# Kernel optimization log

Measured on AMD Instinct MI355X. Metric: run time of the kernel, lower is better.

Reference implementation:

```python
import jax, jax.numpy as jnp
import numpy as np

T = 2048      # num_tokens == max_seq_len
D = 4096      # d_in
H = 32        # num_heads
G = 8         # num_kv_groups
HD = 128      # head_dim
GS = H // G   # group_size = 4
EPS = 1e-6


def _make_rope(t, hd):
    inv_freq = 1.0 / (10000.0 ** (np.arange(0, hd, 2, dtype=np.float64) / hd))
    freqs = np.outer(np.arange(t, dtype=np.float64), inv_freq)      # [T, HD/2]
    emb = np.concatenate([freqs, freqs], axis=-1)                   # [T, HD]
    return (jnp.asarray(np.cos(emb), jnp.float32),
            jnp.asarray(np.sin(emb), jnp.float32))


def setup_inputs() -> dict:
    key = jax.random.key(0)
    ks = jax.random.split(key, 6)
    x = jax.random.normal(ks[0], (T, D), jnp.float32)
    # causal mask: True = masked (upper triangle above diagonal)
    mask = jnp.triu(jnp.ones((T, T), jnp.bool_), k=1)
    cos, sin = _make_rope(T, HD)
    s = 0.02
    Wq = jax.random.normal(ks[1], (D, H * HD), jnp.float32) * s
    Wk = jax.random.normal(ks[2], (D, G * HD), jnp.float32) * s
    Wv = jax.random.normal(ks[3], (D, G * HD), jnp.float32) * s
    Wo = jax.random.normal(ks[4], (H * HD, D), jnp.float32) * s
    qn_w = jnp.ones((HD,), jnp.float32)
    kn_w = jnp.ones((HD,), jnp.float32)
    return {"x": x, "mask": mask, "cos": cos, "sin": sin,
            "Wq": Wq, "Wk": Wk, "Wv": Wv, "Wo": Wo,
            "qn_w": qn_w, "kn_w": kn_w}


def _rmsnorm(u, w):
    # normalize over head_dim (last axis), eps inside sqrt
    var = jnp.mean(jnp.square(u), axis=-1, keepdims=True)
    return u * jax.lax.rsqrt(var + EPS) * w


def _rope(u, cos, sin):
    # rotate-half RoPE; u: [heads, T, HD], cos/sin: [T, HD]
    hd = u.shape[-1]
    u1, u2 = u[..., : hd // 2], u[..., hd // 2:]
    rot = jnp.concatenate([-u2, u1], axis=-1)
    return u * cos[None] + rot * sin[None]


def reference(x, mask, cos, sin, Wq, Wk, Wv, Wo, qn_w, kn_w):
    t = x.shape[0]
    q = (x @ Wq).reshape(t, H, HD).transpose(1, 0, 2)   # [H, T, HD]
    k = (x @ Wk).reshape(t, G, HD).transpose(1, 0, 2)   # [G, T, HD]
    v = (x @ Wv).reshape(t, G, HD).transpose(1, 0, 2)   # [G, T, HD]
    q = _rmsnorm(q, qn_w)
    k = _rmsnorm(k, kn_w)
    q = _rope(q, cos, sin)
    k = _rope(k, cos, sin)
    # GQA expansion: repeat_interleave along head axis
    k = jnp.repeat(k, GS, axis=0)                       # [H, T, HD]
    v = jnp.repeat(v, GS, axis=0)                       # [H, T, HD]
    scores = jnp.einsum('hqd,hkd->hqk', q, k) / (HD ** 0.5)
    scores = jnp.where(mask[None], -jnp.inf, scores)
    w = jax.nn.softmax(scores, axis=-1)
    attn = jnp.einsum('hqk,hkd->hqd', w, v)             # [H, T, HD]
    attn = attn.transpose(1, 0, 2).reshape(t, H * HD)
    return attn @ Wo
```

## Files before the change

kernel.cpp:

```cpp
#include <hip/hip_runtime.h>

#define T_ 2048
#define D_ 4096
#define H_ 32
#define G_ 8
#define HD_ 128

typedef float f32x4 __attribute__((ext_vector_type(4)));
typedef __bf16 bf16x8 __attribute__((ext_vector_type(8)));
typedef unsigned short u16x8 __attribute__((ext_vector_type(8)));
typedef unsigned short u16x4 __attribute__((ext_vector_type(4)));

__device__ __forceinline__ unsigned short f2bf(float f) {
  unsigned u = __builtin_bit_cast(unsigned, f);
  u += 0x7FFFu + ((u >> 16) & 1u);
  return (unsigned short)(u >> 16);
}
__device__ __forceinline__ float bf2f(unsigned short h) {
  return __builtin_bit_cast(float, (unsigned)h << 16);
}

__device__ __forceinline__ void gload_lds16(const unsigned short* g, unsigned short* l) {
  __builtin_amdgcn_global_load_lds((const __attribute__((address_space(1))) void*)g,
                                   (__attribute__((address_space(3))) void*)l, 16, 0, 0);
}

__global__ __launch_bounds__(256) void convert_bf16(const float* __restrict__ in,
                                                    unsigned short* __restrict__ out) {
  const size_t i = ((size_t)blockIdx.x * 256 + threadIdx.x) * 8;
  float4 a = *(const float4*)(in + i);
  float4 b = *(const float4*)(in + i + 4);
  u16x8 o;
  o[0] = f2bf(a.x); o[1] = f2bf(a.y); o[2] = f2bf(a.z); o[3] = f2bf(a.w);
  o[4] = f2bf(b.x); o[5] = f2bf(b.y); o[6] = f2bf(b.z); o[7] = f2bf(b.w);
  *(u16x8*)(out + i) = o;
}

__global__ __launch_bounds__(256) void transpose_convert(const float* __restrict__ Wm,
                                                         unsigned short* __restrict__ Wt,
                                                         int R, int C) {
  __shared__ float tile[64][65];
  const int r0 = blockIdx.x * 64, c0 = blockIdx.y * 64;
  const int lr4 = threadIdx.x >> 6, lc = threadIdx.x & 63;
#pragma unroll
  for (int i = 0; i < 16; ++i) {
    int r = i * 4 + lr4;
    tile[r][lc] = Wm[(size_t)(r0 + r) * C + c0 + lc];
  }
  __syncthreads();
#pragma unroll
  for (int i = 0; i < 16; ++i) {
    int r = i * 4 + lr4;
    Wt[(size_t)(c0 + r) * R + r0 + lc] = f2bf(tile[lc][r]);
  }
}

__global__ __launch_bounds__(256) void transpose_v(const unsigned short* __restrict__ v,
                                                   unsigned short* __restrict__ vt, int stride) {
  __shared__ unsigned short tile[64][65];
  const int t0 = blockIdx.x * 64, d0 = blockIdx.y * 64, g = blockIdx.z;
  const int lr4 = threadIdx.x >> 6, lc = threadIdx.x & 63;
#pragma unroll
  for (int i = 0; i < 16; ++i) {
    int r = i * 4 + lr4;
    tile[r][lc] = v[(size_t)(t0 + r) * stride + g * HD_ + d0 + lc];
  }
  __syncthreads();
#pragma unroll
  for (int i = 0; i < 16; ++i) {
    int r = i * 4 + lr4;
    vt[((size_t)g * HD_ + d0 + r) * T_ + t0 + lc] = tile[lc][r];
  }
}

__global__ __launch_bounds__(256) void norm_rope(const unsigned short* __restrict__ raw,
                                                 int stride,
                                                 unsigned short* __restrict__ outp,
                                                 const float* __restrict__ w,
                                                 const float* __restrict__ cs,
                                                 const float* __restrict__ sn, int NH) {
  const int row = blockIdx.x * 4 + (threadIdx.x >> 6);
  const int lane = threadIdx.x & 63;
  const int t = row / NH, h = row - t * NH;
  const unsigned short* src = raw + (size_t)t * stride + h * HD_;
  float u1 = bf2f(src[lane]);
  float u2 = bf2f(src[lane + 64]);
  float ss = u1 * u1 + u2 * u2;
#pragma unroll
  for (int m = 1; m < 64; m <<= 1) ss += __shfl_xor(ss, m);
  float rr = rsqrtf(ss * (1.f / 128.f) + 1e-6f);
  float c = cs[(size_t)t * HD_ + lane];
  float s = sn[(size_t)t * HD_ + lane];
  float a = u1 * rr * w[lane];
  float b = u2 * rr * w[lane + 64];
  unsigned short* dst = outp + ((size_t)h * T_ + t) * HD_;
  dst[lane]      = f2bf(a * c - b * s);
  dst[lane + 64] = f2bf(b * c + a * s);
}

template <int NF, int F0, int F1>
__device__ __forceinline__ void mfma_g(f32x4 (&acc)[4][NF], bf16x8 (&af)[4][2],
                                       bf16x8 (&bf)[NF][2]) {
  __builtin_amdgcn_s_setprio(1);
#pragma unroll
  for (int fm = 0; fm < 4; ++fm)
#pragma unroll
    for (int fn = F0; fn < F1; ++fn) {
      f32x4 a = acc[fm][fn];
      a = __builtin_amdgcn_mfma_f32_16x16x32_bf16(af[fm][0], bf[fn][0], a, 0, 0, 0);
      a = __builtin_amdgcn_mfma_f32_16x16x32_bf16(af[fm][1], bf[fn][1], a, 0, 0, 0);
      acc[fm][fn] = a;
    }
  __builtin_amdgcn_s_setprio(0);
}

template <int NF, int OUTF32>
__global__ __launch_bounds__(512, 4) void gemm3(const unsigned short* __restrict__ A,
                                                const unsigned short* __restrict__ Bt,
                                                void* __restrict__ Cv, int M, int N,
                                                int K, int LDA) {
  constexpr int BN = NF * 64;
  constexpr int BBUF = NF * 4096;
  __shared__ __align__(16) unsigned short lds[16384 + 2 * BBUF];
  const int tid = threadIdx.x;
  const int wid = tid >> 6, lane = tid & 63;
  const int lr = lane & 15, lhi = lane >> 4;
  const int wr = wid >> 2, wcn = wid & 3;

  int flat = blockIdx.y * gridDim.x + blockIdx.x;
  int nwg = gridDim.x * gridDim.y;
  int swz = (flat & 7) * (nwg >> 3) + (flat >> 3);
  const int brow = (swz & 15) * 128;
  const int bcol = (swz >> 4) * BN;

  const int nt = K >> 6;

  f32x4 acc[4][NF];
#pragma unroll
  for (int b = 0; b < 4; ++b)
#pragma unroll
    for (int c = 0; c < NF; ++c) acc[b][c] = (f32x4){0.f, 0.f, 0.f, 0.f};

  const int t8 = tid >> 3;
  const int srcCol = ((tid & 7) ^ (t8 & 7)) * 8;
  auto stageA = [&](int d, int u, int ktp) {
    gload_lds16(A + (size_t)(brow + u * 64 + t8) * LDA + ktp * 64 + srcCol,
                &lds[d * 8192 + u * 4096 + tid * 8]);
  };
  auto stageB = [&](int d, int v, int ktp) {
    gload_lds16(Bt + (size_t)(bcol + v * 64 + t8) * LDA + ktp * 64 + srcCol,
                &lds[16384 + d * BBUF + v * 4096 + tid * 8]);
  };

  bf16x8 af[4][2], bf[NF][2];
  auto readA = [&](int d) {
#pragma unroll
    for (int fm = 0; fm < 4; ++fm) {
      int row = wr * 64 + fm * 16 + lr;
      int base = d * 8192 + row * 64;
      int sw = (row & 7) << 3;
      af[fm][0] = *(const bf16x8*)&lds[base + ((lhi * 8) ^ sw)];
      af[fm][1] = *(const bf16x8*)&lds[base + ((32 + lhi * 8) ^ sw)];
    }
  };
  auto readBf = [&](int d, int fn, bf16x8 (&slot)[2]) {
    int row = wcn * (16 * NF) + fn * 16 + lr;
    int base = 16384 + d * BBUF + row * 64;
    int sw = (row & 7) << 3;
    slot[0] = *(const bf16x8*)&lds[base + ((lhi * 8) ^ sw)];
    slot[1] = *(const bf16x8*)&lds[base + ((32 + lhi * 8) ^ sw)];
  };

  stageA(0, 0, 0); stageA(0, 1, 0);
#pragma unroll
  for (int v = 0; v < NF; ++v) stageB(0, v, 0);
  stageA(1, 0, 1); stageA(1, 1, 1);
  asm volatile("s_waitcnt vmcnt(2)" ::: "memory");
  __builtin_amdgcn_s_barrier();

  for (int t = 0; t < nt; ++t) {
    const int d = t & 1, dn = d ^ 1;
    if constexpr (NF == 3) {
      readA(d); readBf(d, 0, bf[0]); readBf(d, 1, bf[1]);
      if (t + 1 < nt) { stageB(dn, 0, t + 1); stageB(dn, 1, t + 1); stageB(dn, 2, t + 1); }
      __builtin_amdgcn_s_barrier();
      mfma_g<NF, 0, 2>(acc, af, bf);
      __builtin_amdgcn_s_barrier();
      readBf(d, 2, bf[2]);
      if (t + 2 < nt) { stageA(d, 0, t + 2); stageA(d, 1, t + 2); }
      __builtin_amdgcn_s_barrier();
      mfma_g<NF, 2, 3>(acc, af, bf);
      if (t < nt - 2) asm volatile("s_waitcnt vmcnt(2)" ::: "memory");
      else if (t == nt - 2) asm volatile("s_waitcnt vmcnt(0)" ::: "memory");
      __builtin_amdgcn_s_barrier();
    } else {
      readA(d); readBf(d, 0, bf[0]);
      if (t + 1 < nt) { stageB(dn, 0, t + 1); stageB(dn, 1, t + 1); }
      __builtin_amdgcn_s_barrier();
      mfma_g<NF, 0, 1>(acc, af, bf);
      __builtin_amdgcn_s_barrier();
      readBf(d, 1, bf[1]);
      if (t + 2 < nt) { stageA(d, 0, t + 2); stageA(d, 1, t + 2); }
      __builtin_amdgcn_s_barrier();
      mfma_g<NF, 1, 2>(acc, af, bf);
      if (t < nt - 2) asm volatile("s_waitcnt vmcnt(2)" ::: "memory");
      else if (t == nt - 2) asm volatile("s_waitcnt vmcnt(0)" ::: "memory");
      __builtin_amdgcn_s_barrier();
    }
  }

#pragma unroll
  for (int fm = 0; fm < 4; ++fm)
#pragma unroll
    for (int fn = 0; fn < NF; ++fn) {
      int col = bcol + wcn * (16 * NF) + fn * 16 + lr;
#pragma unroll
      for (int r = 0; r < 4; ++r) {
        int row = brow + wr * 64 + fm * 16 + lhi * 4 + r;
        if (OUTF32)
          ((float*)Cv)[(size_t)row * N + col] = acc[fm][fn][r];
        else
          ((unsigned short*)Cv)[(size_t)row * N + col] = f2bf(acc[fm][fn][r]);
      }
    }
}

__global__ __launch_bounds__(256, 2) void flash_attn(const unsigned short* __restrict__ q,
                                                     const unsigned short* __restrict__ k,
                                                     const unsigned short* __restrict__ vt,
                                                     unsigned short* __restrict__ attnb) {
  const int hp = blockIdx.y;
  const int g = hp >> 1;
  const int h0 = hp * 2;
  const int qc = gridDim.x - 1 - blockIdx.x;
  const int tid = threadIdx.x;
  const int wid = tid >> 6;
  const int lane = tid & 63;
  const int lr = lane & 15, lhi = lane >> 4;
  const int q0 = qc * 64 + wid * 16;

  __shared__ __align__(16) unsigned short Ks[2][64 * HD_];
  __shared__ __align__(16) unsigned short Vs[2][HD_ * 64];
  __shared__ __align__(16) unsigned short p_lds_all[4][2][16 * 64];
  const unsigned short* kg = k + (size_t)g * T_ * HD_;
  const unsigned short* vg = vt + (size_t)g * HD_ * T_;

  int ko[4], vo[4];
#pragma unroll
  for (int p = 0; p < 4; ++p) {
    int ob = (p * 256 + tid) * 16;
    int krow = ob >> 8, kb = ob & 255;
    ko[p] = krow * HD_ + ((kb ^ ((krow & 7) << 4)) >> 1);
    int vrow = ob >> 7, vb2 = ob & 127;
    vo[p] = vrow * T_ + ((vb2 ^ ((vrow & 7) << 4)) >> 1);
  }
  const int lbase = wid * 512;

  const int sx = (lr & 7) << 4;
  const float scale2 = 0.08838834764831845f * 1.4426950408889634f;

  bf16x8 qf0[4], qf1[4];
  {
    const unsigned short* qr0 = q + ((size_t)h0 * T_ + q0 + lr) * HD_ + lhi * 8;
    const unsigned short* qr1 = qr0 + (size_t)T_ * HD_;
#pragma unroll
    for (int c = 0; c < 4; ++c) { qf0[c] = *(const bf16x8*)(qr0 + c * 32);
                                  qf1[c] = *(const bf16x8*)(qr1 + c * 32); }
  }
  f32x4 accO0[8], accO1[8];
#pragma unroll
  for (int i = 0; i < 8; ++i) { accO0[i] = (f32x4){0.f, 0.f, 0.f, 0.f};
                                accO1[i] = (f32x4){0.f, 0.f, 0.f, 0.f}; }
  float mrow0 = -3e38f, mrow1 = -3e38f;
  float lrow0 = 0.f, lrow1 = 0.f;

  const int ntile = qc + 1;

#pragma unroll
  for (int p = 0; p < 4; ++p) {
    gload_lds16(kg + ko[p], &Ks[0][p * 2048 + lbase]);
    gload_lds16(vg + vo[p], &Vs[0][p * 2048 + lbase]);
  }
  __syncthreads();

  for (int kt = 0; kt < ntile; ++kt) {
    const int b = kt & 1;
    const int kv0 = kt << 6;
    if (kt + 1 < ntile) {
      const size_t kofs = (size_t)(kv0 + 64) * HD_;
#pragma unroll
      for (int p = 0; p < 4; ++p) {
        gload_lds16(kg + kofs + ko[p], &Ks[b ^ 1][p * 2048 + lbase]);
        gload_lds16(vg + (kv0 + 64) + vo[p], &Vs[b ^ 1][p * 2048 + lbase]);
      }
    }
    f32x4 st0[4], st1[4];
    __builtin_amdgcn_s_setprio(1);
#pragma unroll
    for (int j = 0; j < 4; ++j) {
      st0[j] = (f32x4){0.f, 0.f, 0.f, 0.f};
      st1[j] = (f32x4){0.f, 0.f, 0.f, 0.f};
      const int krow = j * 16 + lr;
#pragma unroll
      for (int c = 0; c < 4; ++c) {
        bf16x8 kf = *(const bf16x8*)&Ks[b][krow * HD_ + (((c * 64 + lhi * 16) ^ sx) >> 1)];
        st0[j] = __builtin_amdgcn_mfma_f32_16x16x32_bf16(kf, qf0[c], st0[j], 0, 0, 0);
        st1[j] = __builtin_amdgcn_mfma_f32_16x16x32_bf16(kf, qf1[c], st1[j], 0, 0, 0);
      }
    }
    __builtin_amdgcn_s_setprio(0);
    if (kt == ntile - 1) {
#pragma unroll
      for (int j = 0; j < 4; ++j)
#pragma unroll
        for (int r = 0; r < 4; ++r) {
          bool ok = kv0 + j * 16 + lhi * 4 + r <= q0 + lr;
          st0[j][r] = ok ? st0[j][r] * scale2 : -3e38f;
          st1[j][r] = ok ? st1[j][r] * scale2 : -3e38f;
        }
    } else {
#pragma unroll
      for (int j = 0; j < 4; ++j)
#pragma unroll
        for (int r = 0; r < 4; ++r) { st0[j][r] *= scale2; st1[j][r] *= scale2; }
    }
    float pm0 = st0[0][0], pm1 = st1[0][0];
#pragma unroll
    for (int j = 0; j < 4; ++j)
#pragma unroll
      for (int r = 0; r < 4; ++r) { pm0 = fmaxf(pm0, st0[j][r]); pm1 = fmaxf(pm1, st1[j][r]); }
    pm0 = fmaxf(pm0, __shfl_xor(pm0, 16)); pm0 = fmaxf(pm0, __shfl_xor(pm0, 32));
    pm1 = fmaxf(pm1, __shfl_xor(pm1, 16)); pm1 = fmaxf(pm1, __shfl_xor(pm1, 32));
    if (!__all(pm0 - mrow0 <= 8.f)) {
      float mnew = fmaxf(mrow0, pm0);
      float al = __builtin_amdgcn_exp2f(mrow0 - mnew);
      mrow0 = mnew; lrow0 *= al;
      float a0 = __shfl(al, lhi * 4 + 0), a1 = __shfl(al, lhi * 4 + 1);
      float a2 = __shfl(al, lhi * 4 + 2), a3 = __shfl(al, lhi * 4 + 3);
#pragma unroll
      for (int dt = 0; dt < 8; ++dt) {
        accO0[dt][0] *= a0; accO0[dt][1] *= a1; accO0[dt][2] *= a2; accO0[dt][3] *= a3;
      }
    }
    if (!__all(pm1 - mrow1 <= 8.f)) {
      float mnew = fmaxf(mrow1, pm1);
      float al = __builtin_amdgcn_exp2f(mrow1 - mnew);
      mrow1 = mnew; lrow1 *= al;
      float a0 = __shfl(al, lhi * 4 + 0), a1 = __shfl(al, lhi * 4 + 1);
      float a2 = __shfl(al, lhi * 4 + 2), a3 = __shfl(al, lhi * 4 + 3);
#pragma unroll
      for (int dt = 0; dt < 8; ++dt) {
        accO1[dt][0] *= a0; accO1[dt][1] *= a1; accO1[dt][2] *= a2; accO1[dt][3] *= a3;
      }
    }
    float ps0 = 0.f, ps1 = 0.f;
#pragma unroll
    for (int j = 0; j < 4; ++j)
#pragma unroll
      for (int r = 0; r < 4; ++r) {
        float e0 = __builtin_amdgcn_exp2f(st0[j][r] - mrow0);
        float e1 = __builtin_amdgcn_exp2f(st1[j][r] - mrow1);
        st0[j][r] = e0; st1[j][r] = e1;
        ps0 += e0; ps1 += e1;
      }
    ps0 += __shfl_xor(ps0, 16); ps0 += __shfl_xor(ps0, 32);
    ps1 += __shfl_xor(ps1, 16); ps1 += __shfl_xor(ps1, 32);
    lrow0 += ps0; lrow1 += ps1;
    unsigned short* p0 = p_lds_all[wid][0];
    unsigned short* p1 = p_lds_all[wid][1];
#pragma unroll
    for (int j = 0; j < 4; ++j) {
      u16x4 pw0, pw1;
      pw0[0] = f2bf(st0[j][0]); pw0[1] = f2bf(st0[j][1]);
      pw0[2] = f2bf(st0[j][2]); pw0[3] = f2bf(st0[j][3]);
      pw1[0] = f2bf(st1[j][0]); pw1[1] = f2bf(st1[j][1]);
      pw1[2] = f2bf(st1[j][2]); pw1[3] = f2bf(st1[j][3]);
      int off = lr * 64 + (((j * 32 + lhi * 8) ^ sx) >> 1);
      *(u16x4*)&p0[off] = pw0;
      *(u16x4*)&p1[off] = pw1;
    }
    int ra = lr * 64 + (((lhi * 16) ^ sx) >> 1);
    int rb = lr * 64 + (((64 + lhi * 16) ^ sx) >> 1);
    bf16x8 pa00 = *(const bf16x8*)&p0[ra], pa01 = *(const bf16x8*)&p0[rb];
    bf16x8 pa10 = *(const bf16x8*)&p1[ra], pa11 = *(const bf16x8*)&p1[rb];
    __builtin_amdgcn_s_setprio(1);
#pragma unroll
    for (int dt = 0; dt < 8; ++dt) {
      const int vrow = dt * 16 + lr;
      bf16x8 vf0 = *(const bf16x8*)&Vs[b][vrow * 64 + (((lhi * 16) ^ sx) >> 1)];
      bf16x8 vf1 = *(const bf16x8*)&Vs[b][vrow * 64 + (((64 + lhi * 16) ^ sx) >> 1)];
      accO0[dt] = __builtin_amdgcn_mfma_f32_16x16x32_bf16(pa00, vf0, accO0[dt], 0, 0, 0);
      accO0[dt] = __builtin_amdgcn_mfma_f32_16x16x32_bf16(pa01, vf1, accO0[dt], 0, 0, 0);
      accO1[dt] = __builtin_amdgcn_mfma_f32_16x16x32_bf16(pa10, vf0, accO1[dt], 0, 0, 0);
      accO1[dt] = __builtin_amdgcn_mfma_f32_16x16x32_bf16(pa11, vf1, accO1[dt], 0, 0, 0);
    }
    __builtin_amdgcn_s_setprio(0);
    __syncthreads();
  }
  {
    float rinv = 1.f / lrow0;
    float i0 = __shfl(rinv, lhi * 4 + 0), i1 = __shfl(rinv, lhi * 4 + 1);
    float i2 = __shfl(rinv, lhi * 4 + 2), i3 = __shfl(rinv, lhi * 4 + 3);
    float iv[4] = {i0, i1, i2, i3};
#pragma unroll
    for (int r = 0; r < 4; ++r) {
      size_t rowoff = (size_t)(q0 + lhi * 4 + r) * (H_ * HD_) + h0 * HD_;
#pragma unroll
      for (int dt = 0; dt < 8; ++dt) attnb[rowoff + dt * 16 + lr] = f2bf(accO0[dt][r] * iv[r]);
    }
  }
  {
    float rinv = 1.f / lrow1;
    float i0 = __shfl(rinv, lhi * 4 + 0), i1 = __shfl(rinv, lhi * 4 + 1);
    float i2 = __shfl(rinv, lhi * 4 + 2), i3 = __shfl(rinv, lhi * 4 + 3);
    float iv[4] = {i0, i1, i2, i3};
#pragma unroll
    for (int r = 0; r < 4; ++r) {
      size_t rowoff = (size_t)(q0 + lhi * 4 + r) * (H_ * HD_) + (h0 + 1) * HD_;
#pragma unroll
      for (int dt = 0; dt < 8; ++dt) attnb[rowoff + dt * 16 + lr] = f2bf(accO1[dt][r] * iv[r]);
    }
  }
}

extern "C" void kernel_launch(void* const* d_in, const int* in_sizes, int n_in,
                              void* d_out, int out_size, void* d_ws, size_t ws_size,
                              hipStream_t stream) {
  const float* x = (const float*)d_in[0];
  const float* cosT = (const float*)d_in[2];
  const float* sinT = (const float*)d_in[3];
  const float* Wq = (const float*)d_in[4];
  const float* Wk = (const float*)d_in[5];
  const float* Wv = (const float*)d_in[6];
  const float* Wo = (const float*)d_in[7];
  const float* qn = (const float*)d_in[8];
  const float* kn = (const float*)d_in[9];

  unsigned char* w = (unsigned char*)d_ws;
  unsigned short* xb     = (unsigned short*)(w);
  unsigned short* WqkvT  = (unsigned short*)(w + 16777216);
  unsigned short* qkvraw = (unsigned short*)(w + 67108864);
  unsigned short* qbuf   = (unsigned short*)(w + 92274688);
  unsigned short* kbuf   = (unsigned short*)(w + 109051904);
  unsigned short* vtb    = (unsigned short*)(w + 113246208);
  unsigned short* WoT    = WqkvT;
  unsigned short* attnb  = xb;

  convert_bf16<<<dim3(4096), dim3(256), 0, stream>>>(x, xb);
  transpose_convert<<<dim3(64, 64), dim3(256), 0, stream>>>(Wq, WqkvT, 4096, 4096);
  transpose_convert<<<dim3(64, 16), dim3(256), 0, stream>>>(Wk, WqkvT + (size_t)4096 * 4096, 4096, 1024);
  transpose_convert<<<dim3(64, 16), dim3(256), 0, stream>>>(Wv, WqkvT + (size_t)5120 * 4096, 4096, 1024);

  gemm3<3, 0><<<dim3(16, 32), dim3(512), 0, stream>>>(xb, WqkvT, (void*)qkvraw, 2048, 6144, 4096, 4096);

  norm_rope<<<dim3(16384), dim3(256), 0, stream>>>(qkvraw, 6144, qbuf, qn, cosT, sinT, H_);
  norm_rope<<<dim3(4096), dim3(256), 0, stream>>>(qkvraw + 4096, 6144, kbuf, kn, cosT, sinT, G_);
  transpose_v<<<dim3(32, 2, 8), dim3(256), 0, stream>>>(qkvraw + 5120, vtb, 6144);
  transpose_convert<<<dim3(64, 64), dim3(256), 0, stream>>>(Wo, WoT, 4096, 4096);

  flash_attn<<<dim3(32, 16), dim3(256), 0, stream>>>(qbuf, kbuf, vtb, attnb);

  gemm3<2, 1><<<dim3(16, 32), dim3(512), 0, stream>>>(attnb, WoT, d_out, 2048, 4096, 4096, 4096);
}
```

Measured before the change: 355.2 us.

## Use 4-wave GEMM with wider per-wave tiles; remap flash attention to one head per block

```diff
diff --git a/kernel.cpp b/kernel.cpp
--- a/kernel.cpp
+++ b/kernel.cpp
@@ -98,34 +98,36 @@
   dst[lane + 64] = f2bf(b * c + a * s);
 }
 
-template <int NF, int F0, int F1>
-__device__ __forceinline__ void mfma_g(f32x4 (&acc)[4][NF], bf16x8 (&af)[4][2],
-                                       bf16x8 (&bf)[NF][2]) {
+template <int NFW, int HALF>
+__device__ __forceinline__ void mfma_h(f32x4 (&acc)[4][NFW], bf16x8 (&af)[4][2],
+                                       bf16x8 (&bf)[NFW / 2][2]) {
   __builtin_amdgcn_s_setprio(1);
 #pragma unroll
   for (int fm = 0; fm < 4; ++fm)
 #pragma unroll
-    for (int fn = F0; fn < F1; ++fn) {
-      f32x4 a = acc[fm][fn];
-      a = __builtin_amdgcn_mfma_f32_16x16x32_bf16(af[fm][0], bf[fn][0], a, 0, 0, 0);
-      a = __builtin_amdgcn_mfma_f32_16x16x32_bf16(af[fm][1], bf[fn][1], a, 0, 0, 0);
-      acc[fm][fn] = a;
+    for (int j = 0; j < NFW / 2; ++j) {
+      constexpr int base = HALF * (NFW / 2);
+      f32x4 a = acc[fm][base + j];
+      a = __builtin_amdgcn_mfma_f32_16x16x32_bf16(af[fm][0], bf[j][0], a, 0, 0, 0);
+      a = __builtin_amdgcn_mfma_f32_16x16x32_bf16(af[fm][1], bf[j][1], a, 0, 0, 0);
+      acc[fm][base + j] = a;
     }
   __builtin_amdgcn_s_setprio(0);
 }
 
-template <int NF, int OUTF32>
-__global__ __launch_bounds__(512, 4) void gemm3(const unsigned short* __restrict__ A,
+template <int NFW, int OUTF32>
+__global__ __launch_bounds__(256, 2) void gemm4(const unsigned short* __restrict__ A,
                                                 const unsigned short* __restrict__ Bt,
                                                 void* __restrict__ Cv, int M, int N,
                                                 int K, int LDA) {
-  constexpr int BN = NF * 64;
-  constexpr int BBUF = NF * 4096;
-  __shared__ __align__(16) unsigned short lds[16384 + 2 * BBUF];
+  constexpr int BN = 32 * NFW;
+  constexpr int ABUF = 8192;
+  constexpr int BBUF = BN * 64;
+  __shared__ __align__(16) unsigned short lds[2 * ABUF + 2 * BBUF];
   const int tid = threadIdx.x;
   const int wid = tid >> 6, lane = tid & 63;
   const int lr = lane & 15, lhi = lane >> 4;
-  const int wr = wid >> 2, wcn = wid & 3;
+  const int wr = wid >> 1, wcn = wid & 1;
 
   int flat = blockIdx.y * gridDim.x + blockIdx.x;
   int nwg = gridDim.x * gridDim.y;
@@ -135,37 +137,41 @@
 
   const int nt = K >> 6;
 
-  f32x4 acc[4][NF];
+  f32x4 acc[4][NFW];
 #pragma unroll
   for (int b = 0; b < 4; ++b)
 #pragma unroll
-    for (int c = 0; c < NF; ++c) acc[b][c] = (f32x4){0.f, 0.f, 0.f, 0.f};
+    for (int c = 0; c < NFW; ++c) acc[b][c] = (f32x4){0.f, 0.f, 0.f, 0.f};
 
   const int t8 = tid >> 3;
   const int srcCol = ((tid & 7) ^ (t8 & 7)) * 8;
   auto stageA = [&](int d, int u, int ktp) {
-    gload_lds16(A + (size_t)(brow + u * 64 + t8) * LDA + ktp * 64 + srcCol,
-                &lds[d * 8192 + u * 4096 + tid * 8]);
+#pragma unroll
+    for (int l = 0; l < 2; ++l)
+      gload_lds16(A + (size_t)(brow + u * 64 + l * 32 + t8) * LDA + ktp * 64 + srcCol,
+                  &lds[d * ABUF + u * 4096 + l * 2048 + tid * 8]);
   };
   auto stageB = [&](int d, int v, int ktp) {
-    gload_lds16(Bt + (size_t)(bcol + v * 64 + t8) * LDA + ktp * 64 + srcCol,
-                &lds[16384 + d * BBUF + v * 4096 + tid * 8]);
+#pragma unroll
+    for (int l = 0; l < 2; ++l)
+      gload_lds16(Bt + (size_t)(bcol + v * 64 + l * 32 + t8) * LDA + ktp * 64 + srcCol,
+                  &lds[2 * ABUF + d * BBUF + v * 4096 + l * 2048 + tid * 8]);
   };
 
-  bf16x8 af[4][2], bf[NF][2];
+  bf16x8 af[4][2], bf[NFW / 2][2];
   auto readA = [&](int d) {
 #pragma unroll
     for (int fm = 0; fm < 4; ++fm) {
       int row = wr * 64 + fm * 16 + lr;
-      int base = d * 8192 + row * 64;
+      int base = d * ABUF + row * 64;
       int sw = (row & 7) << 3;
       af[fm][0] = *(const bf16x8*)&lds[base + ((lhi * 8) ^ sw)];
       af[fm][1] = *(const bf16x8*)&lds[base + ((32 + lhi * 8) ^ sw)];
     }
   };
   auto readBf = [&](int d, int fn, bf16x8 (&slot)[2]) {
-    int row = wcn * (16 * NF) + fn * 16 + lr;
-    int base = 16384 + d * BBUF + row * 64;
+    int row = wcn * (16 * NFW) + fn * 16 + lr;
+    int base = 2 * ABUF + d * BBUF + row * 64;
     int sw = (row & 7) << 3;
     slot[0] = *(const bf16x8*)&lds[base + ((lhi * 8) ^ sw)];
     slot[1] = *(const bf16x8*)&lds[base + ((32 + lhi * 8) ^ sw)];
@@ -173,47 +179,38 @@
 
   stageA(0, 0, 0); stageA(0, 1, 0);
 #pragma unroll
-  for (int v = 0; v < NF; ++v) stageB(0, v, 0);
+  for (int v = 0; v < NFW / 2; ++v) stageB(0, v, 0);
   stageA(1, 0, 1); stageA(1, 1, 1);
-  asm volatile("s_waitcnt vmcnt(2)" ::: "memory");
+  asm volatile("s_waitcnt vmcnt(4)" ::: "memory");
   __builtin_amdgcn_s_barrier();
 
   for (int t = 0; t < nt; ++t) {
     const int d = t & 1, dn = d ^ 1;
-    if constexpr (NF == 3) {
-      readA(d); readBf(d, 0, bf[0]); readBf(d, 1, bf[1]);
-      if (t + 1 < nt) { stageB(dn, 0, t + 1); stageB(dn, 1, t + 1); stageB(dn, 2, t + 1); }
-      __builtin_amdgcn_s_barrier();
-      mfma_g<NF, 0, 2>(acc, af, bf);
-      __builtin_amdgcn_s_barrier();
-      readBf(d, 2, bf[2]);
-      if (t + 2 < nt) { stageA(d, 0, t + 2); stageA(d, 1, t + 2); }
-      __builtin_amdgcn_s_barrier();
-      mfma_g<NF, 2, 3>(acc, af, bf);
-      if (t < nt - 2) asm volatile("s_waitcnt vmcnt(2)" ::: "memory");
-      else if (t == nt - 2) asm volatile("s_waitcnt vmcnt(0)" ::: "memory");
-      __builtin_amdgcn_s_barrier();
-    } else {
-      readA(d); readBf(d, 0, bf[0]);
-      if (t + 1 < nt) { stageB(dn, 0, t + 1); stageB(dn, 1, t + 1); }
-      __builtin_amdgcn_s_barrier();
-      mfma_g<NF, 0, 1>(acc, af, bf);
-      __builtin_amdgcn_s_barrier();
-      readBf(d, 1, bf[1]);
-      if (t + 2 < nt) { stageA(d, 0, t + 2); stageA(d, 1, t + 2); }
-      __builtin_amdgcn_s_barrier();
-      mfma_g<NF, 1, 2>(acc, af, bf);
-      if (t < nt - 2) asm volatile("s_waitcnt vmcnt(2)" ::: "memory");
-      else if (t == nt - 2) asm volatile("s_waitcnt vmcnt(0)" ::: "memory");
-      __builtin_amdgcn_s_barrier();
-    }
+    readA(d);
+#pragma unroll
+    for (int j = 0; j < NFW / 2; ++j) readBf(d, j, bf[j]);
+    if (t + 1 < nt) {
+#pragma unroll
+      for (int v = 0; v < NFW / 2; ++v) stageB(dn, v, t + 1);
+    }
+    __builtin_amdgcn_s_barrier();
+    mfma_h<NFW, 0>(acc, af, bf);
+    __builtin_amdgcn_s_barrier();
+#pragma unroll
+    for (int j = 0; j < NFW / 2; ++j) readBf(d, NFW / 2 + j, bf[j]);
+    if (t + 2 < nt) { stageA(d, 0, t + 2); stageA(d, 1, t + 2); }
+    __builtin_amdgcn_s_barrier();
+    mfma_h<NFW, 1>(acc, af, bf);
+    if (t < nt - 2) asm volatile("s_waitcnt vmcnt(4)" ::: "memory");
+    else if (t == nt - 2) asm volatile("s_waitcnt vmcnt(0)" ::: "memory");
+    __builtin_amdgcn_s_barrier();
   }
 
 #pragma unroll
   for (int fm = 0; fm < 4; ++fm)
 #pragma unroll
-    for (int fn = 0; fn < NF; ++fn) {
-      int col = bcol + wcn * (16 * NF) + fn * 16 + lr;
+    for (int fn = 0; fn < NFW; ++fn) {
+      int col = bcol + wcn * (16 * NFW) + fn * 16 + lr;
 #pragma unroll
       for (int r = 0; r < 4; ++r) {
         int row = brow + wr * 64 + fm * 16 + lhi * 4 + r;
@@ -229,15 +226,14 @@
                                                      const unsigned short* __restrict__ k,
                                                      const unsigned short* __restrict__ vt,
                                                      unsigned short* __restrict__ attnb) {
-  const int hp = blockIdx.y;
-  const int g = hp >> 1;
-  const int h0 = hp * 2;
+  const int h = blockIdx.y;
+  const int g = h >> 2;
   const int qc = gridDim.x - 1 - blockIdx.x;
   const int tid = threadIdx.x;
   const int wid = tid >> 6;
   const int lane = tid & 63;
   const int lr = lane & 15, lhi = lane >> 4;
-  const int q0 = qc * 64 + wid * 16;
+  const int q0 = qc * 128 + wid * 32;
 
   __shared__ __align__(16) unsigned short Ks[2][64 * HD_];
   __shared__ __align__(16) unsigned short Vs[2][HD_ * 64];
@@ -254,15 +250,14 @@
     int vrow = ob >> 7, vb2 = ob & 127;
     vo[p] = vrow * T_ + ((vb2 ^ ((vrow & 7) << 4)) >> 1);
   }
-  const int lbase = wid * 512;
 
   const int sx = (lr & 7) << 4;
   const float scale2 = 0.08838834764831845f * 1.4426950408889634f;
 
   bf16x8 qf0[4], qf1[4];
   {
-    const unsigned short* qr0 = q + ((size_t)h0 * T_ + q0 + lr) * HD_ + lhi * 8;
-    const unsigned short* qr1 = qr0 + (size_t)T_ * HD_;
+    const unsigned short* qr0 = q + ((size_t)h * T_ + q0 + lr) * HD_ + lhi * 8;
+    const unsigned short* qr1 = qr0 + (size_t)16 * HD_;
 #pragma unroll
     for (int c = 0; c < 4; ++c) { qf0[c] = *(const bf16x8*)(qr0 + c * 32);
                                   qf1[c] = *(const bf16x8*)(qr1 + c * 32); }
@@ -274,12 +269,12 @@
   float mrow0 = -3e38f, mrow1 = -3e38f;
   float lrow0 = 0.f, lrow1 = 0.f;
 
-  const int ntile = qc + 1;
+  const int ntile = 2 * qc + 2;
 
 #pragma unroll
   for (int p = 0; p < 4; ++p) {
-    gload_lds16(kg + ko[p], &Ks[0][p * 2048 + lbase]);
-    gload_lds16(vg + vo[p], &Vs[0][p * 2048 + lbase]);
+    gload_lds16(kg + ko[p], &Ks[0][p * 2048 + tid * 8]);
+    gload_lds16(vg + vo[p], &Vs[0][p * 2048 + tid * 8]);
   }
   __syncthreads();
 
@@ -290,8 +285,8 @@
       const size_t kofs = (size_t)(kv0 + 64) * HD_;
 #pragma unroll
       for (int p = 0; p < 4; ++p) {
-        gload_lds16(kg + kofs + ko[p], &Ks[b ^ 1][p * 2048 + lbase]);
-        gload_lds16(vg + (kv0 + 64) + vo[p], &Vs[b ^ 1][p * 2048 + lbase]);
+        gload_lds16(kg + kofs + ko[p], &Ks[b ^ 1][p * 2048 + tid * 8]);
+        gload_lds16(vg + (kv0 + 64) + vo[p], &Vs[b ^ 1][p * 2048 + tid * 8]);
       }
     }
     f32x4 st0[4], st1[4];
@@ -309,14 +304,14 @@
       }
     }
     __builtin_amdgcn_s_setprio(0);
-    if (kt == ntile - 1) {
+    if (((kt + 1) << 6) > q0 + 1) {
 #pragma unroll
       for (int j = 0; j < 4; ++j)
 #pragma unroll
         for (int r = 0; r < 4; ++r) {
-          bool ok = kv0 + j * 16 + lhi * 4 + r <= q0 + lr;
-          st0[j][r] = ok ? st0[j][r] * scale2 : -3e38f;
-          st1[j][r] = ok ? st1[j][r] * scale2 : -3e38f;
+          int kidx = kv0 + j * 16 + lhi * 4 + r;
+          st0[j][r] = (kidx <= q0 + lr)      ? st0[j][r] * scale2 : -3e38f;
+          st1[j][r] = (kidx <= q0 + 16 + lr) ? st1[j][r] * scale2 : -3e38f;
         }
     } else {
 #pragma unroll
@@ -404,7 +399,7 @@
     float iv[4] = {i0, i1, i2, i3};
 #pragma unroll
     for (int r = 0; r < 4; ++r) {
-      size_t rowoff = (size_t)(q0 + lhi * 4 + r) * (H_ * HD_) + h0 * HD_;
+      size_t rowoff = (size_t)(q0 + lhi * 4 + r) * (H_ * HD_) + h * HD_;
 #pragma unroll
       for (int dt = 0; dt < 8; ++dt) attnb[rowoff + dt * 16 + lr] = f2bf(accO0[dt][r] * iv[r]);
     }
@@ -416,7 +411,7 @@
     float iv[4] = {i0, i1, i2, i3};
 #pragma unroll
     for (int r = 0; r < 4; ++r) {
-      size_t rowoff = (size_t)(q0 + lhi * 4 + r) * (H_ * HD_) + (h0 + 1) * HD_;
+      size_t rowoff = (size_t)(q0 + 16 + lhi * 4 + r) * (H_ * HD_) + h * HD_;
 #pragma unroll
       for (int dt = 0; dt < 8; ++dt) attnb[rowoff + dt * 16 + lr] = f2bf(accO1[dt][r] * iv[r]);
     }
@@ -451,14 +446,14 @@
   transpose_convert<<<dim3(64, 16), dim3(256), 0, stream>>>(Wk, WqkvT + (size_t)4096 * 4096, 4096, 1024);
   transpose_convert<<<dim3(64, 16), dim3(256), 0, stream>>>(Wv, WqkvT + (size_t)5120 * 4096, 4096, 1024);
 
-  gemm3<3, 0><<<dim3(16, 32), dim3(512), 0, stream>>>(xb, WqkvT, (void*)qkvraw, 2048, 6144, 4096, 4096);
+  gemm4<6, 0><<<dim3(16, 32), dim3(256), 0, stream>>>(xb, WqkvT, (void*)qkvraw, 2048, 6144, 4096, 4096);
 
   norm_rope<<<dim3(16384), dim3(256), 0, stream>>>(qkvraw, 6144, qbuf, qn, cosT, sinT, H_);
   norm_rope<<<dim3(4096), dim3(256), 0, stream>>>(qkvraw + 4096, 6144, kbuf, kn, cosT, sinT, G_);
   transpose_v<<<dim3(32, 2, 8), dim3(256), 0, stream>>>(qkvraw + 5120, vtb, 6144);
   transpose_convert<<<dim3(64, 64), dim3(256), 0, stream>>>(Wo, WoT, 4096, 4096);
 
-  flash_attn<<<dim3(32, 16), dim3(256), 0, stream>>>(qbuf, kbuf, vtb, attnb);
-
-  gemm3<2, 1><<<dim3(16, 32), dim3(512), 0, stream>>>(attnb, WoT, d_out, 2048, 4096, 4096, 4096);
-}
+  flash_attn<<<dim3(16, 32), dim3(256), 0, stream>>>(qbuf, kbuf, vtb, attnb);
+
+  gemm4<4, 1><<<dim3(16, 32), dim3(256), 0, stream>>>(attnb, WoT, d_out, 2048, 4096, 4096, 4096);
+}
```

New measurement: 344.2 us. 1.03x faster.
